# Kernel optimization log

Measured on AMD Instinct MI355X. Metric: run time of the kernel, lower is better.

Reference implementation:

```python
import jax, jax.numpy as jnp
import numpy as np

N_DET = 32

def _nuc_features(nuc_coords, nuc_charges, nuc_mask):
    # masked mean-centering of nuclear coords, then concat charge feature
    m = nuc_mask[:, None].astype(nuc_coords.dtype)  # [n_nuc, 1]
    mean = (nuc_coords * m).sum(0, keepdims=True) / jnp.maximum(m.sum(0, keepdims=True), 1.0)
    centered = nuc_coords - mean
    feats = jnp.concatenate([nuc_charges[:, None], centered], axis=-1)  # [n_nuc, 4]
    return feats * m

def _spin_orbitals(e_coords, e_mask, nuc_coords, feats, nuc_mask, W_pi, W_zeta):
    # exponent factors / nuclear weights via per-nucleus linear maps, then transpose
    zeta = (feats @ W_pi).T   # exponent_factors [n_det*max_e, n_nuc]
    pi = (feats @ W_zeta).T   # nuclear_weights  [n_det*max_e, n_nuc]
    # masked pairwise electron-nucleus distances
    diff = e_coords[:, None, :] - nuc_coords[None, :, :]          # [n_e, n_nuc, 3]
    dist_mask = e_mask[:, None] & nuc_mask[None, :]               # [n_e, n_nuc]
    d2 = (diff * diff).sum(-1)
    dist = jnp.sqrt(jnp.where(dist_mask, d2, 1.0))                # safe sqrt on masked entries
    # exp-decay envelope, masked, weighted sum over nuclei
    expo = jnp.where(dist_mask[:, None, :],
                     jnp.exp(-jnp.abs(dist[:, None, :] * zeta[None])), 0.0)  # [n_e, nd*me, n_nuc]
    orb = (pi[None] * expo).sum(-1)                               # [n_e, nd*me]
    n_e = e_coords.shape[0]
    orb = orb.reshape(n_e, N_DET, -1).swapaxes(-2, -3)            # [n_det, n_e, max_e]
    sm = e_mask[:, None] & e_mask[None, :]
    return jnp.where(sm, orb, jnp.eye(n_e, dtype=orb.dtype))


def setup_inputs() -> dict:
    key = jax.random.key(0)
    ks = jax.random.split(key, 8)
    ME, MN = 128, 128
    f = jnp.float32
    return {
        "up_coords": jax.random.normal(ks[0], (ME, 3), f),
        "down_coords": jax.random.normal(ks[1], (ME, 3), f),
        "nuc_coords": jax.random.normal(ks[2], (MN, 3), f),
        "nuc_charges": jax.random.uniform(ks[3], (MN,), f),
        "W_pi_up": jax.random.normal(ks[4], (4, N_DET * ME), f),
        "W_zeta_up": jax.random.normal(ks[5], (4, N_DET * ME), f),
        "W_pi_down": jax.random.normal(ks[6], (4, N_DET * ME), f),
        "W_zeta_down": jax.random.normal(ks[7], (4, N_DET * ME), f),
        "up_mask": jnp.ones((ME,), bool),
        "down_mask": jnp.ones((ME,), bool),
        "nuc_mask": jnp.ones((MN,), bool),
    }


def reference(up_coords, down_coords, nuc_coords, nuc_charges,
              W_pi_up, W_zeta_up, W_pi_down, W_zeta_down,
              up_mask, down_mask, nuc_mask):
    feats = _nuc_features(nuc_coords, nuc_charges, nuc_mask)
    up = _spin_orbitals(up_coords, up_mask, nuc_coords, feats, nuc_mask, W_pi_up, W_zeta_up)
    down = _spin_orbitals(down_coords, down_mask, nuc_coords, feats, nuc_mask, W_pi_down, W_zeta_down)
    return jnp.stack([up, down])  # [2, n_det, n_e, max_e]
```

## Files before the change

kernel.cpp:

```cpp
#include <hip/hip_runtime.h>
#include <cstddef>

#define NDET 32
#define ME   128
#define MN   128
#define NOUT (NDET * ME)
#define LOG2E 1.4426950408889634f

#if __has_builtin(__builtin_amdgcn_exp2f)
#define EXP2(x) __builtin_amdgcn_exp2f(x)
#else
#define EXP2(x) exp2f(x)
#endif

__global__ __launch_bounds__(256) void env_kernel(
    const float* __restrict__ up_coords,
    const float* __restrict__ down_coords,
    const float* __restrict__ nuc_coords,
    const float* __restrict__ nuc_charges,
    const float* __restrict__ W_pi_up,
    const float* __restrict__ W_zeta_up,
    const float* __restrict__ W_pi_down,
    const float* __restrict__ W_zeta_down,
    float* __restrict__ out)
{
    __shared__ float4 feats4[MN];
    __shared__ float4 duv[MN * 2];

    const int tid = (int)threadIdx.x;
    const int e0  = (int)blockIdx.x * 8;
    const int d   = (int)blockIdx.y;
    const int s   = (int)blockIdx.z;

    const float* ec = s ? down_coords : up_coords;
    const float* We = s ? W_pi_down   : W_pi_up;
    const float* Ww = s ? W_zeta_down : W_zeta_up;

    if (tid < MN) {
        feats4[tid] = make_float4(nuc_charges[tid],
                                  nuc_coords[tid * 3 + 0],
                                  nuc_coords[tid * 3 + 1],
                                  nuc_coords[tid * 3 + 2]);
    }
    __syncthreads();

    float mx = 0.f, my = 0.f, mz = 0.f;
    #pragma unroll 8
    for (int n = 0; n < MN; ++n) {
        float4 f = feats4[n];
        mx += f.y; my += f.z; mz += f.w;
    }
    mx *= (1.f / MN); my *= (1.f / MN); mz *= (1.f / MN);

    {
        const int n  = tid >> 1;
        const int gb = tid & 1;
        const float4 f = feats4[n];
        float r0, r1, r2, r3;
        {
            const int e = e0 + gb * 4 + 0;
            float dx = ec[e*3+0] - f.y, dy = ec[e*3+1] - f.z, dz = ec[e*3+2] - f.w;
            r0 = sqrtf(fmaf(dx, dx, fmaf(dy, dy, dz * dz))) * LOG2E;
        }
        {
            const int e = e0 + gb * 4 + 1;
            float dx = ec[e*3+0] - f.y, dy = ec[e*3+1] - f.z, dz = ec[e*3+2] - f.w;
            r1 = sqrtf(fmaf(dx, dx, fmaf(dy, dy, dz * dz))) * LOG2E;
        }
        {
            const int e = e0 + gb * 4 + 2;
            float dx = ec[e*3+0] - f.y, dy = ec[e*3+1] - f.z, dz = ec[e*3+2] - f.w;
            r2 = sqrtf(fmaf(dx, dx, fmaf(dy, dy, dz * dz))) * LOG2E;
        }
        {
            const int e = e0 + gb * 4 + 3;
            float dx = ec[e*3+0] - f.y, dy = ec[e*3+1] - f.z, dz = ec[e*3+2] - f.w;
            r3 = sqrtf(fmaf(dx, dx, fmaf(dy, dy, dz * dz))) * LOG2E;
        }
        duv[n * 2 + gb] = make_float4(r0, r1, r2, r3);
    }
    __syncthreads();

    if (tid < MN) {
        float4 f = feats4[tid];
        feats4[tid] = make_float4(f.x, f.y - mx, f.z - my, f.w - mz);
    }
    __syncthreads();

    const int j = tid & 127;
    const int g = tid >> 7;
    const int o = d * ME + j;

    const float we0 = We[0*NOUT+o], we1 = We[1*NOUT+o], we2 = We[2*NOUT+o], we3 = We[3*NOUT+o];
    const float ww0 = Ww[0*NOUT+o], ww1 = Ww[1*NOUT+o], ww2 = Ww[2*NOUT+o], ww3 = Ww[3*NOUT+o];

    float a0 = 0.f, a1 = 0.f, a2 = 0.f, a3 = 0.f;
    #pragma unroll 4
    for (int n = 0; n < MN; ++n) {
        const float4 f = feats4[n];
        const float zeta = fmaf(f.x, we0, fmaf(f.y, we1, fmaf(f.z, we2, f.w * we3)));
        const float pi   = fmaf(f.x, ww0, fmaf(f.y, ww1, fmaf(f.z, ww2, f.w * ww3)));
        const float az = __builtin_fabsf(zeta);
        const float4 du = duv[n * 2 + g];
        a0 = fmaf(pi, EXP2(-du.x * az), a0);
        a1 = fmaf(pi, EXP2(-du.y * az), a1);
        a2 = fmaf(pi, EXP2(-du.z * az), a2);
        a3 = fmaf(pi, EXP2(-du.w * az), a3);
    }

    const int e_base = e0 + g * 4;
    float* op = out + ((((size_t)s * NDET + d) * ME + e_base) * ME + j);
    op[0]      = a0;
    op[ME]     = a1;
    op[2 * ME] = a2;
    op[3 * ME] = a3;
}

extern "C" void kernel_launch(void* const* d_in, const int* in_sizes, int n_in,
                              void* d_out, int out_size, void* d_ws, size_t ws_size,
                              hipStream_t stream)
{
    (void)in_sizes; (void)n_in; (void)out_size; (void)d_ws; (void)ws_size;
    env_kernel<<<dim3(16, 32, 2), 256, 0, stream>>>(
        (const float*)d_in[0],
        (const float*)d_in[1],
        (const float*)d_in[2],
        (const float*)d_in[3],
        (const float*)d_in[4],
        (const float*)d_in[5],
        (const float*)d_in[6],
        (const float*)d_in[7],
        (float*)d_out);
}
```

Baseline: 98.68 us.

## Process 16 electrons per block and parallelize nuclear mean reduction

Each block now handles 16 electrons instead of 8, so each thread accumulates 8 outputs and reuses its zeta/pi computation across twice as many exponentials. The grid is halved accordingly. Electron coordinates are staged in shared memory, and the per-thread serial 128-element mean loop is replaced with a wavefront shuffle reduction. The trade-off is fewer blocks (512) for the GPU and more registers per thread.

```diff
diff --git a/kernel.cpp b/kernel.cpp
--- a/kernel.cpp
+++ b/kernel.cpp
@@ -25,10 +25,12 @@
     float* __restrict__ out)
 {
     __shared__ float4 feats4[MN];
-    __shared__ float4 duv[MN * 2];
+    __shared__ float  duv[MN * 16];
+    __shared__ float  ecl[16 * 3];
+    __shared__ float  msum[2][3];
 
     const int tid = (int)threadIdx.x;
-    const int e0  = (int)blockIdx.x * 8;
+    const int e0  = (int)blockIdx.x * 16;
     const int d   = (int)blockIdx.y;
     const int s   = (int)blockIdx.z;
 
@@ -41,43 +43,47 @@
                                   nuc_coords[tid * 3 + 0],
                                   nuc_coords[tid * 3 + 1],
                                   nuc_coords[tid * 3 + 2]);
+    } else if (tid < MN + 48) {
+        ecl[tid - MN] = ec[e0 * 3 + (tid - MN)];
     }
     __syncthreads();
 
-    float mx = 0.f, my = 0.f, mz = 0.f;
-    #pragma unroll 8
-    for (int n = 0; n < MN; ++n) {
-        float4 f = feats4[n];
-        mx += f.y; my += f.z; mz += f.w;
+    if (tid < MN) {
+        float4 f = feats4[tid];
+        float sx = f.y, sy = f.z, sz = f.w;
+        #pragma unroll
+        for (int off = 32; off > 0; off >>= 1) {
+            sx += __shfl_xor(sx, off);
+            sy += __shfl_xor(sy, off);
+            sz += __shfl_xor(sz, off);
+        }
+        if ((tid & 63) == 0) {
+            const int w = tid >> 6;
+            msum[w][0] = sx; msum[w][1] = sy; msum[w][2] = sz;
+        }
     }
-    mx *= (1.f / MN); my *= (1.f / MN); mz *= (1.f / MN);
+    __syncthreads();
+
+    const float mx = (msum[0][0] + msum[1][0]) * (1.f / MN);
+    const float my = (msum[0][1] + msum[1][1]) * (1.f / MN);
+    const float mz = (msum[0][2] + msum[1][2]) * (1.f / MN);
 
     {
-        const int n  = tid >> 1;
-        const int gb = tid & 1;
+        const int n = tid >> 1;
+        const int h = tid & 1;
         const float4 f = feats4[n];
-        float r0, r1, r2, r3;
-        {
-            const int e = e0 + gb * 4 + 0;
-            float dx = ec[e*3+0] - f.y, dy = ec[e*3+1] - f.z, dz = ec[e*3+2] - f.w;
-            r0 = sqrtf(fmaf(dx, dx, fmaf(dy, dy, dz * dz))) * LOG2E;
+        float r[8];
+        #pragma unroll
+        for (int i = 0; i < 8; ++i) {
+            const int e = h * 8 + i;
+            const float dx = ecl[e * 3 + 0] - f.y;
+            const float dy = ecl[e * 3 + 1] - f.z;
+            const float dz = ecl[e * 3 + 2] - f.w;
+            r[i] = sqrtf(fmaf(dx, dx, fmaf(dy, dy, dz * dz))) * LOG2E;
         }
-        {
-            const int e = e0 + gb * 4 + 1;
-            float dx = ec[e*3+0] - f.y, dy = ec[e*3+1] - f.z, dz = ec[e*3+2] - f.w;
-            r1 = sqrtf(fmaf(dx, dx, fmaf(dy, dy, dz * dz))) * LOG2E;
-        }
-        {
-            const int e = e0 + gb * 4 + 2;
-            float dx = ec[e*3+0] - f.y, dy = ec[e*3+1] - f.z, dz = ec[e*3+2] - f.w;
-            r2 = sqrtf(fmaf(dx, dx, fmaf(dy, dy, dz * dz))) * LOG2E;
-        }
-        {
-            const int e = e0 + gb * 4 + 3;
-            float dx = ec[e*3+0] - f.y, dy = ec[e*3+1] - f.z, dz = ec[e*3+2] - f.w;
-            r3 = sqrtf(fmaf(dx, dx, fmaf(dy, dy, dz * dz))) * LOG2E;
-        }
-        duv[n * 2 + gb] = make_float4(r0, r1, r2, r3);
+        float4* dst = (float4*)&duv[n * 16 + h * 8];
+        dst[0] = make_float4(r[0], r[1], r[2], r[3]);
+        dst[1] = make_float4(r[4], r[5], r[6], r[7]);
     }
     __syncthreads();
 
@@ -95,25 +101,37 @@
     const float ww0 = Ww[0*NOUT+o], ww1 = Ww[1*NOUT+o], ww2 = Ww[2*NOUT+o], ww3 = Ww[3*NOUT+o];
 
     float a0 = 0.f, a1 = 0.f, a2 = 0.f, a3 = 0.f;
-    #pragma unroll 4
+    float a4 = 0.f, a5 = 0.f, a6 = 0.f, a7 = 0.f;
+
+    const float4* du4 = (const float4*)duv;
+    #pragma unroll 2
     for (int n = 0; n < MN; ++n) {
         const float4 f = feats4[n];
         const float zeta = fmaf(f.x, we0, fmaf(f.y, we1, fmaf(f.z, we2, f.w * we3)));
         const float pi   = fmaf(f.x, ww0, fmaf(f.y, ww1, fmaf(f.z, ww2, f.w * ww3)));
         const float az = __builtin_fabsf(zeta);
-        const float4 du = duv[n * 2 + g];
-        a0 = fmaf(pi, EXP2(-du.x * az), a0);
-        a1 = fmaf(pi, EXP2(-du.y * az), a1);
-        a2 = fmaf(pi, EXP2(-du.z * az), a2);
-        a3 = fmaf(pi, EXP2(-du.w * az), a3);
+        const float4 u0 = du4[n * 4 + g * 2 + 0];
+        const float4 u1 = du4[n * 4 + g * 2 + 1];
+        a0 = fmaf(pi, EXP2(-(u0.x * az)), a0);
+        a1 = fmaf(pi, EXP2(-(u0.y * az)), a1);
+        a2 = fmaf(pi, EXP2(-(u0.z * az)), a2);
+        a3 = fmaf(pi, EXP2(-(u0.w * az)), a3);
+        a4 = fmaf(pi, EXP2(-(u1.x * az)), a4);
+        a5 = fmaf(pi, EXP2(-(u1.y * az)), a5);
+        a6 = fmaf(pi, EXP2(-(u1.z * az)), a6);
+        a7 = fmaf(pi, EXP2(-(u1.w * az)), a7);
     }
 
-    const int e_base = e0 + g * 4;
+    const int e_base = e0 + g * 8;
     float* op = out + ((((size_t)s * NDET + d) * ME + e_base) * ME + j);
-    op[0]      = a0;
-    op[ME]     = a1;
+    op[0 * ME] = a0;
+    op[1 * ME] = a1;
     op[2 * ME] = a2;
     op[3 * ME] = a3;
+    op[4 * ME] = a4;
+    op[5 * ME] = a5;
+    op[6 * ME] = a6;
+    op[7 * ME] = a7;
 }
 
 extern "C" void kernel_launch(void* const* d_in, const int* in_sizes, int n_in,
@@ -121,7 +139,7 @@
                               hipStream_t stream)
 {
     (void)in_sizes; (void)n_in; (void)out_size; (void)d_ws; (void)ws_size;
-    env_kernel<<<dim3(16, 32, 2), 256, 0, stream>>>(
+    env_kernel<<<dim3(8, 32, 2), 256, 0, stream>>>(
         (const float*)d_in[0],
         (const float*)d_in[1],
         (const float*)d_in[2],
```

Result: faster. 93.71 us (-5.0%).
